# Kernel optimization log

Measured on AMD Instinct MI355X. Metric: run time of the kernel, lower is better.

The kernel has to match this reference:

```python
import jax, jax.numpy as jnp
import numpy as np

B, D, H = 4096, 64, 1024  # batch, state dim, hidden width


def setup_inputs() -> dict:
    key = jax.random.key(0)
    ks = jax.random.split(key, 4)
    def w(k, shape, fan_in):
        return (jax.random.normal(k, shape, jnp.float32) / np.float32(np.sqrt(fan_in)))
    return {
        "x": jax.random.normal(ks[0], (B, 1 + D), jnp.float32),
        "W1": w(ks[1], (D, H), D),
        "b1": jnp.zeros((H,), jnp.float32),
        "W2": w(ks[2], (H, H), H),
        "b2": jnp.zeros((H,), jnp.float32),
        "W3": w(ks[3], (H, D), H),
        "b3": jnp.zeros((D,), jnp.float32),
    }


def _mlp(z, W1, b1, W2, b2, W3, b3):
    # tanh MLP vector field: d -> h -> h -> d
    h = jnp.tanh(z @ W1 + b1)
    h = jnp.tanh(h @ W2 + b2)
    return h @ W3 + b3


def reference(x, W1, b1, W2, b2, W3, b3):
    x_in = x[:, 1:]                        # [B, D] state (col 0 is logp channel)
    f = lambda z: _mlp(z, W1, b1, W2, b2, W3, b3)
    x_out = f(x_in)                        # [B, D]

    # Exact Jacobian trace: same math as the torch per-dim autograd.grad loop,
    # expressed as D forward-mode JVPs vmapped over the identity basis.
    eye = jnp.eye(x_in.shape[1], dtype=x.dtype)

    def diag_entry(e):                     # e: [D] basis vector
        _, t = jax.jvp(f, (x_in,), (jnp.broadcast_to(e, x_in.shape),))
        return t @ e                       # [B] = J[:, i, i]

    trJ = jnp.sum(jax.vmap(diag_entry)(eye), axis=0)  # [B]

    out = jnp.concatenate([-trJ[:, None], x_out], axis=1)  # [B, 1+D]
    return out + 0.0 * x  # faithful to `+ 0 * x` in the original
```

## Files before the change

### kernel.cpp

```cpp
#include <hip/hip_runtime.h>
#include <cmath>

typedef unsigned short u16;
typedef __attribute__((ext_vector_type(8))) short s8v;
typedef __attribute__((ext_vector_type(4))) float f4v;
typedef __attribute__((ext_vector_type(16))) float f16v;

__device__ __forceinline__ u16 f2bf(float f) {
    union { float f; unsigned u; } v; v.f = f;
    unsigned r = v.u + 0x7FFFu + ((v.u >> 16) & 1u);
    return (u16)(r >> 16);
}
__device__ __forceinline__ float tanh_fast(float x) {
    float e = __builtin_amdgcn_exp2f(x * 2.88539008177792681f);
    return 1.f - 2.f * __builtin_amdgcn_rcpf(1.f + e);
}
__device__ __forceinline__ int wslot(int row, int c) {
    return ((((c >> 2) << 6) | ((c & 3) << 4) | (row & 15)) ^ c);
}
__device__ __forceinline__ size_t fragoff(int n, int k) {
    return (((size_t)(n >> 5) * 64 + (k >> 4)) * 64 + (n & 31) + (((k >> 3) & 1) << 5)) * 8 + (k & 7);
}

__launch_bounds__(256)
__global__ void cnf_prep(const float* __restrict__ x, const float* __restrict__ W1,
                         const float* __restrict__ W2, const float* __restrict__ W3,
                         u16* __restrict__ W2Tf, u16* __restrict__ VTf,
                         u16* __restrict__ xb, u16* __restrict__ W1T,
                         u16* __restrict__ W3Tf, float* __restrict__ trJ)
{
    __shared__ float w2s[32][33];
    __shared__ float w1s[32][68];
    const int a = blockIdx.x * 32;
    const int b = blockIdx.y * 32;
    const int t = threadIdx.x;

    #pragma unroll
    for (int it = 0; it < 4; ++it) {
        int idx = t + it * 256;
        w2s[idx >> 5][idx & 31] = W2[(a + (idx >> 5)) * 1024 + b + (idx & 31)];
    }
    #pragma unroll
    for (int it = 0; it < 8; ++it) {
        int idx = t + it * 256;
        w1s[idx & 31][idx >> 5] = W1[(idx >> 5) * 1024 + a + (idx & 31)];
    }
    __syncthreads();

    #pragma unroll
    for (int it = 0; it < 4; ++it) {
        int idx = t + it * 256;
        int rr = idx >> 5, cc = idx & 31;
        W2Tf[fragoff(b + rr, a + cc)] = f2bf(w2s[cc][rr]);
    }
    #pragma unroll
    for (int it = 0; it < 4; ++it) {
        int idx = t + it * 256;
        int qq = idx >> 5, pp = idx & 31;
        const float* w3row = W3 + (b + qq) * 64;
        float u = 0.f;
        #pragma unroll
        for (int i4 = 0; i4 < 16; ++i4) {
            f4v wv  = *(const f4v*)&w1s[pp][i4 * 4];
            f4v w3v = *(const f4v*)&w3row[i4 * 4];
            u += wv[0]*w3v[0] + wv[1]*w3v[1] + wv[2]*w3v[2] + wv[3]*w3v[3];
        }
        VTf[fragoff(b + qq, a + pp)] = f2bf(w2s[pp][qq] * u);
    }
    {
        int bid = blockIdx.y * 32 + blockIdx.x;
        int e = bid * 256 + t;
        xb[e] = f2bf(x[(e >> 6) * 65 + 1 + (e & 63)]);
    }
    if (blockIdx.y == 0) {
        int pp = t >> 3, i0 = (t & 7) * 8;
        s8v v;
        #pragma unroll
        for (int j = 0; j < 8; ++j) v[j] = (short)f2bf(w1s[pp][i0 + j]);
        *(s8v*)&W1T[(a + pp) * 64 + i0] = v;
        if (t < 128) trJ[blockIdx.x * 128 + t] = 0.f;
    }
    if (blockIdx.y == 1) {
        int idx = blockIdx.x * 256 + t;
        int n = idx & 63, k0 = (idx >> 6) * 8;
        s8v v;
        #pragma unroll
        for (int j = 0; j < 8; ++j) v[j] = (short)f2bf(W3[(k0 + j) * 64 + n]);
        *(s8v*)&W3Tf[fragoff(n, k0)] = v;
    }
}

__launch_bounds__(256)
__global__ void cnf_gemm1(const u16* __restrict__ xb, const u16* __restrict__ W1T,
                          const float* __restrict__ b1,
                          u16* __restrict__ h1, u16* __restrict__ g1)
{
    __shared__ __align__(16) u16 lds[12 * 1024];
    const int t = threadIdx.x;
    const int wave = t >> 6, lane = t & 63;
    const int wm = wave >> 1, wn = wave & 1;
    const int g = lane >> 4, lr = lane & 15;
    const int arow0 = blockIdx.x * 128, bcol0 = blockIdx.y * 64;

    #pragma unroll
    for (int i = 0; i < 4; ++i) {
        int ch = t + i * 256, row = ch >> 3, c = ch & 7;
        *(s8v*)&lds[(row >> 4) * 1024 + wslot(row, c) * 8] =
            *(const s8v*)&xb[(arow0 + row) * 64 + c * 8];
    }
    #pragma unroll
    for (int i = 0; i < 2; ++i) {
        int ch = t + i * 256, row = ch >> 3, c = ch & 7;
        *(s8v*)&lds[(8 + (row >> 4)) * 1024 + wslot(row, c) * 8] =
            *(const s8v*)&W1T[(bcol0 + row) * 64 + c * 8];
    }
    __syncthreads();

    f4v acc[4][2];
    #pragma unroll
    for (int mi = 0; mi < 4; ++mi)
        #pragma unroll
        for (int ni = 0; ni < 2; ++ni) acc[mi][ni] = f4v{0.f,0.f,0.f,0.f};

    #pragma unroll
    for (int ks = 0; ks < 2; ++ks) {
        const int lo = (ks * 64 + (lane ^ ((ks * 4 + g) & 7))) * 8;
        s8v af[4], bf[2];
        #pragma unroll
        for (int mi = 0; mi < 4; ++mi) af[mi] = *(const s8v*)&lds[(wm * 4 + mi) * 1024 + lo];
        #pragma unroll
        for (int ni = 0; ni < 2; ++ni) bf[ni] = *(const s8v*)&lds[(8 + wn * 2 + ni) * 1024 + lo];
        #pragma unroll
        for (int mi = 0; mi < 4; ++mi)
            #pragma unroll
            for (int ni = 0; ni < 2; ++ni)
                acc[mi][ni] = __builtin_amdgcn_mfma_f32_16x16x32_bf16(af[mi], bf[ni], acc[mi][ni], 0, 0, 0);
    }

    #pragma unroll
    for (int mi = 0; mi < 4; ++mi) {
        const int rowb = arow0 + wm * 64 + mi * 16 + g * 4;
        #pragma unroll
        for (int ni = 0; ni < 2; ++ni) {
            const int col = bcol0 + wn * 32 + ni * 16 + lr;
            const float bv = b1[col];
            #pragma unroll
            for (int r = 0; r < 4; ++r) {
                float h = tanh_fast(acc[mi][ni][r] + bv);
                h1[(rowb + r) * 1024 + col] = f2bf(h);
                g1[(rowb + r) * 1024 + col] = f2bf(1.f - h * h);
            }
        }
    }
}

#define LOADA(d0, d1, d2, d3, ko)                                              \
    do { d0 = *(const s8v*)(h1p0 + (ko)); d1 = *(const s8v*)(h1p1 + (ko));     \
         d2 = *(const s8v*)(g1p0 + (ko)); d3 = *(const s8v*)(g1p1 + (ko)); } while (0)

#define LOADB(B, kkg)                                                          \
    do { _Pragma("unroll")                                                     \
         for (int _ks = 0; _ks < 2; ++_ks)                                     \
         _Pragma("unroll")                                                     \
         for (int _ni = 0; _ni < 2; ++_ni) {                                   \
             size_t _o = (((size_t)(ntb + wn * 2 + _ni) * 64 + (kkg)*2 + _ks) * 64 + lane) * 8; \
             B[_ks*4 + _ni*2 + 0] = *(const s8v*)&W2Tf[_o];                    \
             B[_ks*4 + _ni*2 + 1] = *(const s8v*)&VTf[_o];                     \
         } } while (0)

#define WRITEA(s0, s1, s2, s3, bb)                                             \
    do { u16* _wb = &lds[bb][0];                                               \
         *(s8v*)&_wb[sdst0] = s0; *(s8v*)&_wb[sdst1] = s1;                     \
         *(s8v*)&_wb[4096 + sdst0] = s2; *(s8v*)&_wb[4096 + sdst1] = s3; } while (0)

#define MIDBODY(kt, Aw0, Aw1, Aw2, Aw3, Al0, Al1, Al2, Al3, Bc, Bn)            \
    {                                                                          \
        if ((kt) < 30) { const int _ko = ((kt) + 2) * 32;                      \
                         LOADA(Al0, Al1, Al2, Al3, _ko); }                     \
        if ((kt) < 31) { WRITEA(Aw0, Aw1, Aw2, Aw3, ((kt) + 1) & 1);           \
                         LOADB(Bn, (kt) + 1); }                                \
        const u16* buf = &lds[(kt) & 1][0];                                    \
        _Pragma("unroll")                                                      \
        for (int ks = 0; ks < 2; ++ks) {                                       \
            const int lp = (lane ^ ((lane >> 5) << 2) ^ (ks << 1)) * 8;        \
            s8v af1[2], af2[2];                                                \
            _Pragma("unroll")                                                  \
            for (int mi = 0; mi < 2; ++mi) {                                   \
                int R = (wm * 2 + mi) * 2 + ks;                                \
                af1[mi] = *(const s8v*)&buf[R * 512 + lp];                     \
                af2[mi] = *(const s8v*)&buf[4096 + R * 512 + lp];              \
            }                                                                  \
            _Pragma("unroll")                                                  \
            for (int mi = 0; mi < 2; ++mi)                                     \
                _Pragma("unroll")                                              \
                for (int ni = 0; ni < 2; ++ni) {                               \
                    acc1[mi][ni] = __builtin_amdgcn_mfma_f32_32x32x16_bf16(af1[mi], Bc[ks*4+ni*2+0], acc1[mi][ni], 0, 0, 0); \
                    acc2[mi][ni] = __builtin_amdgcn_mfma_f32_32x32x16_bf16(af2[mi], Bc[ks*4+ni*2+1], acc2[mi][ni], 0, 0, 0); \
                }                                                              \
        }                                                                      \
        __syncthreads();                                                       \
    }

__launch_bounds__(256, 1)
__global__ void cnf_mid(const u16* __restrict__ h1, const u16* __restrict__ g1,
                        const u16* __restrict__ W2Tf, const u16* __restrict__ VTf,
                        const float* __restrict__ b2,
                        u16* __restrict__ h2f, float* __restrict__ trJ)
{
    __shared__ __align__(16) u16 lds[2][8192];

    const int t = threadIdx.x;
    const int wave = t >> 6, lane = t & 63;
    const int wm = wave >> 1, wn = wave & 1;
    const int arow0 = blockIdx.x * 128;
    const int ntb = blockIdx.y * 4;

    const int row0 = t >> 2,        c0 = t & 3;
    const int row1 = (t + 256) >> 2, c1 = t & 3;
    int R0 = (row0 >> 5) * 2 + (c0 >> 1), L0 = (row0 & 31) + ((c0 & 1) << 5);
    int R1 = (row1 >> 5) * 2 + (c1 >> 1), L1 = (row1 & 31) + ((c1 & 1) << 5);
    const int sdst0 = (R0 * 64 + (L0 ^ ((L0 >> 5) << 2) ^ ((R0 & 1) << 1))) * 8;
    const int sdst1 = (R1 * 64 + (L1 ^ ((L1 >> 5) << 2) ^ ((R1 & 1) << 1))) * 8;
    const u16* h1p0 = h1 + (size_t)(arow0 + row0) * 1024 + c0 * 8;
    const u16* h1p1 = h1 + (size_t)(arow0 + row1) * 1024 + c1 * 8;
    const u16* g1p0 = g1 + (size_t)(arow0 + row0) * 1024 + c0 * 8;
    const u16* g1p1 = g1 + (size_t)(arow0 + row1) * 1024 + c1 * 8;

    f16v acc1[2][2], acc2[2][2];
    #pragma unroll
    for (int mi = 0; mi < 2; ++mi)
        #pragma unroll
        for (int ni = 0; ni < 2; ++ni) {
            #pragma unroll
            for (int r = 0; r < 16; ++r) { acc1[mi][ni][r] = 0.f; acc2[mi][ni][r] = 0.f; }
        }

    s8v aA0, aA1, aA2, aA3, aB0, aB1, aB2, aB3;
    s8v bA[8], bB[8];

    LOADA(aA0, aA1, aA2, aA3, 0);
    WRITEA(aA0, aA1, aA2, aA3, 0);
    LOADA(aB0, aB1, aB2, aB3, 32);
    LOADB(bA, 0);
    __syncthreads();

    for (int kt2 = 0; kt2 < 16; ++kt2) {
        const int kt = kt2 * 2;
        MIDBODY(kt,     aB0, aB1, aB2, aB3, aA0, aA1, aA2, aA3, bA, bB);
        MIDBODY(kt + 1, aA0, aA1, aA2, aA3, aB0, aB1, aB2, aB3, bB, bA);
    }

    const int l31 = lane & 31, lh = lane >> 5;
    #pragma unroll
    for (int mi = 0; mi < 2; ++mi) {
        const int rt = (arow0 >> 5) + wm * 2 + mi;
        float tr[16];
        #pragma unroll
        for (int r = 0; r < 16; ++r) tr[r] = 0.f;
        #pragma unroll
        for (int ni = 0; ni < 2; ++ni) {
            const int q0 = (ntb + wn * 2 + ni) * 32;
            const float bv = b2[q0 + l31];
            const size_t hb = (((size_t)rt * 64 + ((q0 + l31) >> 4)) * 64
                               + (((l31 >> 3) & 1) << 5)) * 8 + (l31 & 7) + lh * 32;
            #pragma unroll
            for (int r = 0; r < 16; ++r) {
                float hh = tanh_fast(acc1[mi][ni][r] + bv);
                float gg = 1.f - hh * hh;
                h2f[hb + ((r & 3) + ((r >> 2) << 3)) * 8] = f2bf(hh);
                tr[r] += acc2[mi][ni][r] * gg;
            }
        }
        #pragma unroll
        for (int off = 1; off < 32; off <<= 1)
            #pragma unroll
            for (int r = 0; r < 16; ++r) tr[r] += __shfl_xor(tr[r], off);
        if (l31 == 0) {
            const int rowb = arow0 + wm * 64 + mi * 32 + lh * 4;
            #pragma unroll
            for (int r = 0; r < 16; ++r)
                atomicAdd(&trJ[rowb + (r & 3) + ((r >> 2) << 3)], tr[r]);
        }
    }
}

__launch_bounds__(256)
__global__ void cnf_out(const u16* __restrict__ h2f, const u16* __restrict__ W3Tf,
                        const float* __restrict__ b3, const float* __restrict__ trJ,
                        float* __restrict__ out)
{
    __shared__ float red[4][32][64];
    const int t = threadIdx.x;
    const int wave = t >> 6, lane = t & 63;
    const int rt = blockIdx.x;

    f16v acc[2];
    #pragma unroll
    for (int ni = 0; ni < 2; ++ni)
        #pragma unroll
        for (int r = 0; r < 16; ++r) acc[ni][r] = 0.f;

    #pragma unroll
    for (int kki = 0; kki < 16; ++kki) {
        const int kk = wave * 16 + kki;
        s8v af = *(const s8v*)&h2f[(((size_t)rt * 64 + kk) * 64 + lane) * 8];
        #pragma unroll
        for (int ni = 0; ni < 2; ++ni) {
            s8v bf = *(const s8v*)&W3Tf[(((size_t)ni * 64 + kk) * 64 + lane) * 8];
            acc[ni] = __builtin_amdgcn_mfma_f32_32x32x16_bf16(af, bf, acc[ni], 0, 0, 0);
        }
    }
    const int l31 = lane & 31, lh = lane >> 5;
    #pragma unroll
    for (int ni = 0; ni < 2; ++ni)
        #pragma unroll
        for (int r = 0; r < 16; ++r)
            red[wave][(r & 3) + ((r >> 2) << 3) + lh * 4][ni * 32 + l31] = acc[ni][r];
    __syncthreads();

    #pragma unroll
    for (int i = 0; i < 8; ++i) {
        int o = t * 8 + i;
        int row = o >> 6, col = o & 63;
        float s = red[0][row][col] + red[1][row][col] + red[2][row][col] + red[3][row][col] + b3[col];
        out[(size_t)(rt * 32 + row) * 65 + 1 + col] = s;
    }
    if (t < 32) out[(size_t)(rt * 32 + t) * 65] = -trJ[rt * 32 + t];
}

extern "C" void kernel_launch(void* const* d_in, const int* in_sizes, int n_in,
                              void* d_out, int out_size, void* d_ws, size_t ws_size,
                              hipStream_t stream) {
    const float* x  = (const float*)d_in[0];
    const float* W1 = (const float*)d_in[1];
    const float* b1 = (const float*)d_in[2];
    const float* W2 = (const float*)d_in[3];
    const float* b2 = (const float*)d_in[4];
    const float* W3 = (const float*)d_in[5];
    const float* b3 = (const float*)d_in[6];
    float* out = (float*)d_out;

    char* ws = (char*)d_ws;
    u16*   h1b = (u16*)(ws);
    u16*   g1b = (u16*)(ws + (size_t)( 8u << 20));
    u16*   h2f = (u16*)(ws + (size_t)(16u << 20));
    u16*   W2T = (u16*)(ws + (size_t)(24u << 20));
    u16*   VTb = (u16*)(ws + (size_t)(26u << 20));
    float* trJ = (float*)(ws + (size_t)(28u << 20));
    u16*   xbb = (u16*)(ws + (size_t)(28u << 20) + 65536);
    u16*   W1T = (u16*)(ws + (size_t)(28u << 20) + 65536 + 524288);
    u16*   W3T = (u16*)(ws + (size_t)(28u << 20) + 65536 + 524288 + 131072);

    cnf_prep <<<dim3(32, 32), 256, 0, stream>>>(x, W1, W2, W3, W2T, VTb, xbb, W1T, W3T, trJ);
    cnf_gemm1<<<dim3(32, 16), 256, 0, stream>>>(xbb, W1T, b1, h1b, g1b);
    cnf_mid  <<<dim3(32, 8),  256, 0, stream>>>(h1b, g1b, W2T, VTb, b2, h2f, trJ);
    cnf_out  <<<128,          256, 0, stream>>>(h2f, W3T, b3, trJ, out);
}
```

Measured before the change: 61.29 us.

## Store h1/g1 in MFMA fragment layout and drop LDS staging in mid GEMM

gemm1 now stages its tanh outputs in swizzled LDS and writes h1/g1 to global memory in pre-tiled MFMA fragment order with 16-byte vector stores, replacing scalar row-major stores. cnf_mid then loads A and B fragments straight from global memory each k-step, with no LDS double buffering and no barriers. The aim is to cut LDS traffic and sync overhead in the main GEMM and to make the gemm1 stores coalesced. The cost is that mid no longer prefetches explicitly, so it depends on cache hits and compiler scheduling (unroll 4) to hide global load latency.

```diff
diff --git a/kernel.cpp b/kernel.cpp
--- a/kernel.cpp
+++ b/kernel.cpp
@@ -93,9 +93,11 @@
 __launch_bounds__(256)
 __global__ void cnf_gemm1(const u16* __restrict__ xb, const u16* __restrict__ W1T,
                           const float* __restrict__ b1,
-                          u16* __restrict__ h1, u16* __restrict__ g1)
+                          u16* __restrict__ h1f, u16* __restrict__ g1f)
 {
     __shared__ __align__(16) u16 lds[12 * 1024];
+    __shared__ __align__(16) u16 hls[128 * 64];
+    __shared__ __align__(16) u16 gls[128 * 64];
     const int t = threadIdx.x;
     const int wave = t >> 6, lane = t & 63;
     const int wm = wave >> 1, wn = wave & 1;
@@ -139,115 +141,94 @@
 
     #pragma unroll
     for (int mi = 0; mi < 4; ++mi) {
-        const int rowb = arow0 + wm * 64 + mi * 16 + g * 4;
+        const int rowl = wm * 64 + mi * 16 + g * 4;
         #pragma unroll
         for (int ni = 0; ni < 2; ++ni) {
-            const int col = bcol0 + wn * 32 + ni * 16 + lr;
-            const float bv = b1[col];
+            const int coll = wn * 32 + ni * 16 + lr;
+            const float bv = b1[bcol0 + coll];
+            const int cc = coll >> 3, jj = coll & 7;
             #pragma unroll
             for (int r = 0; r < 4; ++r) {
+                const int row = rowl + r;
                 float h = tanh_fast(acc[mi][ni][r] + bv);
-                h1[(rowb + r) * 1024 + col] = f2bf(h);
-                g1[(rowb + r) * 1024 + col] = f2bf(1.f - h * h);
+                int idx = row * 64 + ((cc ^ (row & 7)) << 3) + jj;
+                hls[idx] = f2bf(h);
+                gls[idx] = f2bf(1.f - h * h);
             }
         }
     }
-}
-
-#define LOADA(d0, d1, d2, d3, ko)                                              \
-    do { d0 = *(const s8v*)(h1p0 + (ko)); d1 = *(const s8v*)(h1p1 + (ko));     \
-         d2 = *(const s8v*)(g1p0 + (ko)); d3 = *(const s8v*)(g1p1 + (ko)); } while (0)
-
-#define LOADB(B, kkg)                                                          \
-    do { _Pragma("unroll")                                                     \
-         for (int _ks = 0; _ks < 2; ++_ks)                                     \
-         _Pragma("unroll")                                                     \
-         for (int _ni = 0; _ni < 2; ++_ni) {                                   \
-             size_t _o = (((size_t)(ntb + wn * 2 + _ni) * 64 + (kkg)*2 + _ks) * 64 + lane) * 8; \
-             B[_ks*4 + _ni*2 + 0] = *(const s8v*)&W2Tf[_o];                    \
-             B[_ks*4 + _ni*2 + 1] = *(const s8v*)&VTf[_o];                     \
-         } } while (0)
-
-#define WRITEA(s0, s1, s2, s3, bb)                                             \
-    do { u16* _wb = &lds[bb][0];                                               \
-         *(s8v*)&_wb[sdst0] = s0; *(s8v*)&_wb[sdst1] = s1;                     \
-         *(s8v*)&_wb[4096 + sdst0] = s2; *(s8v*)&_wb[4096 + sdst1] = s3; } while (0)
-
-#define MIDBODY(kt, Aw0, Aw1, Aw2, Aw3, Al0, Al1, Al2, Al3, Bc, Bn)            \
-    {                                                                          \
-        if ((kt) < 30) { const int _ko = ((kt) + 2) * 32;                      \
-                         LOADA(Al0, Al1, Al2, Al3, _ko); }                     \
-        if ((kt) < 31) { WRITEA(Aw0, Aw1, Aw2, Aw3, ((kt) + 1) & 1);           \
-                         LOADB(Bn, (kt) + 1); }                                \
-        const u16* buf = &lds[(kt) & 1][0];                                    \
-        _Pragma("unroll")                                                      \
-        for (int ks = 0; ks < 2; ++ks) {                                       \
-            const int lp = (lane ^ ((lane >> 5) << 2) ^ (ks << 1)) * 8;        \
-            s8v af1[2], af2[2];                                                \
-            _Pragma("unroll")                                                  \
-            for (int mi = 0; mi < 2; ++mi) {                                   \
-                int R = (wm * 2 + mi) * 2 + ks;                                \
-                af1[mi] = *(const s8v*)&buf[R * 512 + lp];                     \
-                af2[mi] = *(const s8v*)&buf[4096 + R * 512 + lp];              \
-            }                                                                  \
-            _Pragma("unroll")                                                  \
-            for (int mi = 0; mi < 2; ++mi)                                     \
-                _Pragma("unroll")                                              \
-                for (int ni = 0; ni < 2; ++ni) {                               \
-                    acc1[mi][ni] = __builtin_amdgcn_mfma_f32_32x32x16_bf16(af1[mi], Bc[ks*4+ni*2+0], acc1[mi][ni], 0, 0, 0); \
-                    acc2[mi][ni] = __builtin_amdgcn_mfma_f32_32x32x16_bf16(af2[mi], Bc[ks*4+ni*2+1], acc2[mi][ni], 0, 0, 0); \
-                }                                                              \
-        }                                                                      \
-        __syncthreads();                                                       \
-    }
+    __syncthreads();
+
+    const int rt0 = arow0 >> 5, kk0 = bcol0 >> 4;
+    #pragma unroll
+    for (int i = 0; i < 4; ++i) {
+        const int tile = (i * 256 + t) >> 6;
+        const int ln = t & 63;
+        const int rt = tile >> 2, kk = tile & 3;
+        const int row = rt * 32 + (ln & 31);
+        const int kb = kk * 16 + (ln >> 5) * 8;
+        const int src = row * 64 + (((kb >> 3) ^ (row & 7)) << 3);
+        const size_t dst = ((size_t)(rt0 + rt) * 64 + (kk0 + kk)) * 512 + ln * 8;
+        *(s8v*)&h1f[dst] = *(const s8v*)&hls[src];
+        *(s8v*)&g1f[dst] = *(const s8v*)&gls[src];
+    }
+}
 
 __launch_bounds__(256, 1)
-__global__ void cnf_mid(const u16* __restrict__ h1, const u16* __restrict__ g1,
+__global__ void cnf_mid(const u16* __restrict__ h1f, const u16* __restrict__ g1f,
                         const u16* __restrict__ W2Tf, const u16* __restrict__ VTf,
                         const float* __restrict__ b2,
                         u16* __restrict__ h2f, float* __restrict__ trJ)
 {
-    __shared__ __align__(16) u16 lds[2][8192];
-
     const int t = threadIdx.x;
     const int wave = t >> 6, lane = t & 63;
     const int wm = wave >> 1, wn = wave & 1;
     const int arow0 = blockIdx.x * 128;
     const int ntb = blockIdx.y * 4;
-
-    const int row0 = t >> 2,        c0 = t & 3;
-    const int row1 = (t + 256) >> 2, c1 = t & 3;
-    int R0 = (row0 >> 5) * 2 + (c0 >> 1), L0 = (row0 & 31) + ((c0 & 1) << 5);
-    int R1 = (row1 >> 5) * 2 + (c1 >> 1), L1 = (row1 & 31) + ((c1 & 1) << 5);
-    const int sdst0 = (R0 * 64 + (L0 ^ ((L0 >> 5) << 2) ^ ((R0 & 1) << 1))) * 8;
-    const int sdst1 = (R1 * 64 + (L1 ^ ((L1 >> 5) << 2) ^ ((R1 & 1) << 1))) * 8;
-    const u16* h1p0 = h1 + (size_t)(arow0 + row0) * 1024 + c0 * 8;
-    const u16* h1p1 = h1 + (size_t)(arow0 + row1) * 1024 + c1 * 8;
-    const u16* g1p0 = g1 + (size_t)(arow0 + row0) * 1024 + c0 * 8;
-    const u16* g1p1 = g1 + (size_t)(arow0 + row1) * 1024 + c1 * 8;
+    const int rt0 = (arow0 >> 5) + wm * 2;
+    const int nt0 = ntb + wn * 2;
+
+    const u16* pa1[2], *pa2[2], *pb1[2], *pb2[2];
+    #pragma unroll
+    for (int mi = 0; mi < 2; ++mi) {
+        pa1[mi] = h1f + (size_t)(rt0 + mi) * 64 * 512 + lane * 8;
+        pa2[mi] = g1f + (size_t)(rt0 + mi) * 64 * 512 + lane * 8;
+    }
+    #pragma unroll
+    for (int ni = 0; ni < 2; ++ni) {
+        pb1[ni] = W2Tf + (size_t)(nt0 + ni) * 64 * 512 + lane * 8;
+        pb2[ni] = VTf  + (size_t)(nt0 + ni) * 64 * 512 + lane * 8;
+    }
 
     f16v acc1[2][2], acc2[2][2];
     #pragma unroll
     for (int mi = 0; mi < 2; ++mi)
         #pragma unroll
+        for (int ni = 0; ni < 2; ++ni)
+            #pragma unroll
+            for (int r = 0; r < 16; ++r) { acc1[mi][ni][r] = 0.f; acc2[mi][ni][r] = 0.f; }
+
+    #pragma unroll 4
+    for (int kk = 0; kk < 64; ++kk) {
+        const size_t o = (size_t)kk * 512;
+        s8v a1[2], a2[2], b1f[2], b2f[2];
+        #pragma unroll
+        for (int mi = 0; mi < 2; ++mi) {
+            a1[mi] = *(const s8v*)(pa1[mi] + o);
+            a2[mi] = *(const s8v*)(pa2[mi] + o);
+        }
+        #pragma unroll
         for (int ni = 0; ni < 2; ++ni) {
-            #pragma unroll
-            for (int r = 0; r < 16; ++r) { acc1[mi][ni][r] = 0.f; acc2[mi][ni][r] = 0.f; }
-        }
-
-    s8v aA0, aA1, aA2, aA3, aB0, aB1, aB2, aB3;
-    s8v bA[8], bB[8];
-
-    LOADA(aA0, aA1, aA2, aA3, 0);
-    WRITEA(aA0, aA1, aA2, aA3, 0);
-    LOADA(aB0, aB1, aB2, aB3, 32);
-    LOADB(bA, 0);
-    __syncthreads();
-
-    for (int kt2 = 0; kt2 < 16; ++kt2) {
-        const int kt = kt2 * 2;
-        MIDBODY(kt,     aB0, aB1, aB2, aB3, aA0, aA1, aA2, aA3, bA, bB);
-        MIDBODY(kt + 1, aA0, aA1, aA2, aA3, aB0, aB1, aB2, aB3, bB, bA);
+            b1f[ni] = *(const s8v*)(pb1[ni] + o);
+            b2f[ni] = *(const s8v*)(pb2[ni] + o);
+        }
+        #pragma unroll
+        for (int mi = 0; mi < 2; ++mi)
+            #pragma unroll
+            for (int ni = 0; ni < 2; ++ni) {
+                acc1[mi][ni] = __builtin_amdgcn_mfma_f32_32x32x16_bf16(a1[mi], b1f[ni], acc1[mi][ni], 0, 0, 0);
+                acc2[mi][ni] = __builtin_amdgcn_mfma_f32_32x32x16_bf16(a2[mi], b2f[ni], acc2[mi][ni], 0, 0, 0);
+            }
     }
 
     const int l31 = lane & 31, lh = lane >> 5;
@@ -341,8 +322,8 @@
     float* out = (float*)d_out;
 
     char* ws = (char*)d_ws;
-    u16*   h1b = (u16*)(ws);
-    u16*   g1b = (u16*)(ws + (size_t)( 8u << 20));
+    u16*   h1f = (u16*)(ws);
+    u16*   g1f = (u16*)(ws + (size_t)( 8u << 20));
     u16*   h2f = (u16*)(ws + (size_t)(16u << 20));
     u16*   W2T = (u16*)(ws + (size_t)(24u << 20));
     u16*   VTb = (u16*)(ws + (size_t)(26u << 20));
@@ -352,7 +333,7 @@
     u16*   W3T = (u16*)(ws + (size_t)(28u << 20) + 65536 + 524288 + 131072);
 
     cnf_prep <<<dim3(32, 32), 256, 0, stream>>>(x, W1, W2, W3, W2T, VTb, xbb, W1T, W3T, trJ);
-    cnf_gemm1<<<dim3(32, 16), 256, 0, stream>>>(xbb, W1T, b1, h1b, g1b);
-    cnf_mid  <<<dim3(32, 8),  256, 0, stream>>>(h1b, g1b, W2T, VTb, b2, h2f, trJ);
+    cnf_gemm1<<<dim3(32, 16), 256, 0, stream>>>(xbb, W1T, b1, h1f, g1f);
+    cnf_mid  <<<dim3(32, 8),  256, 0, stream>>>(h1f, g1f, W2T, VTb, b2, h2f, trJ);
     cnf_out  <<<128,          256, 0, stream>>>(h2f, W3T, b3, trJ, out);
 }
```

Measured after the change: 65.47 us. +6.8%, slower.

## Split mid GEMM across 8 waves, stage gemm1 epilogue in LDS, fix prep layout

Applied to the files above, without the earlier changes.

The mid kernel moves from 4 waves of 256 threads, each owning a 2x2 tile of 32x32 MFMA blocks, to 8 waves of 512 threads, each owning a 1x2 tile. This halves accumulator registers per wave and allows two blocks per CU (launch bounds 512,2), trading fewer registers per wave for more latency hiding. gemm1 now writes h1/g1 into swizzled LDS first and then stores 16-byte vectors, replacing scattered 2-byte global stores. The prep kernel's W1 shared tile is transposed to a padded [64][33] layout to cut bank conflicts, at the cost of replacing vector LDS reads with scalar ones.

```diff
diff --git a/kernel.cpp b/kernel.cpp
--- a/kernel.cpp
+++ b/kernel.cpp
@@ -30,7 +30,7 @@
                          u16* __restrict__ W3Tf, float* __restrict__ trJ)
 {
     __shared__ float w2s[32][33];
-    __shared__ float w1s[32][68];
+    __shared__ float w1s[64][33];
     const int a = blockIdx.x * 32;
     const int b = blockIdx.y * 32;
     const int t = threadIdx.x;
@@ -43,7 +43,7 @@
     #pragma unroll
     for (int it = 0; it < 8; ++it) {
         int idx = t + it * 256;
-        w1s[idx & 31][idx >> 5] = W1[(idx >> 5) * 1024 + a + (idx & 31)];
+        w1s[idx >> 5][idx & 31] = W1[(idx >> 5) * 1024 + a + (idx & 31)];
     }
     __syncthreads();
 
@@ -61,9 +61,9 @@
         float u = 0.f;
         #pragma unroll
         for (int i4 = 0; i4 < 16; ++i4) {
-            f4v wv  = *(const f4v*)&w1s[pp][i4 * 4];
             f4v w3v = *(const f4v*)&w3row[i4 * 4];
-            u += wv[0]*w3v[0] + wv[1]*w3v[1] + wv[2]*w3v[2] + wv[3]*w3v[3];
+            u += w3v[0] * w1s[i4 * 4 + 0][pp] + w3v[1] * w1s[i4 * 4 + 1][pp]
+               + w3v[2] * w1s[i4 * 4 + 2][pp] + w3v[3] * w1s[i4 * 4 + 3][pp];
         }
         VTf[fragoff(b + qq, a + pp)] = f2bf(w2s[pp][qq] * u);
     }
@@ -76,7 +76,7 @@
         int pp = t >> 3, i0 = (t & 7) * 8;
         s8v v;
         #pragma unroll
-        for (int j = 0; j < 8; ++j) v[j] = (short)f2bf(w1s[pp][i0 + j]);
+        for (int j = 0; j < 8; ++j) v[j] = (short)f2bf(w1s[i0 + j][pp]);
         *(s8v*)&W1T[(a + pp) * 64 + i0] = v;
         if (t < 128) trJ[blockIdx.x * 128 + t] = 0.f;
     }
@@ -96,6 +96,8 @@
                           u16* __restrict__ h1, u16* __restrict__ g1)
 {
     __shared__ __align__(16) u16 lds[12 * 1024];
+    __shared__ __align__(16) u16 hls[128 * 64];
+    __shared__ __align__(16) u16 gls[128 * 64];
     const int t = threadIdx.x;
     const int wave = t >> 6, lane = t & 63;
     const int wm = wave >> 1, wn = wave & 1;
@@ -139,69 +141,73 @@
 
     #pragma unroll
     for (int mi = 0; mi < 4; ++mi) {
-        const int rowb = arow0 + wm * 64 + mi * 16 + g * 4;
+        const int rowl = wm * 64 + mi * 16 + g * 4;
         #pragma unroll
         for (int ni = 0; ni < 2; ++ni) {
-            const int col = bcol0 + wn * 32 + ni * 16 + lr;
-            const float bv = b1[col];
+            const int coll = wn * 32 + ni * 16 + lr;
+            const float bv = b1[bcol0 + coll];
+            const int cc = coll >> 3, jj = coll & 7;
             #pragma unroll
             for (int r = 0; r < 4; ++r) {
+                const int row = rowl + r;
                 float h = tanh_fast(acc[mi][ni][r] + bv);
-                h1[(rowb + r) * 1024 + col] = f2bf(h);
-                g1[(rowb + r) * 1024 + col] = f2bf(1.f - h * h);
+                int idx = row * 64 + ((cc ^ (row & 7)) << 3) + jj;
+                hls[idx] = f2bf(h);
+                gls[idx] = f2bf(1.f - h * h);
             }
         }
     }
-}
-
-#define LOADA(d0, d1, d2, d3, ko)                                              \
-    do { d0 = *(const s8v*)(h1p0 + (ko)); d1 = *(const s8v*)(h1p1 + (ko));     \
-         d2 = *(const s8v*)(g1p0 + (ko)); d3 = *(const s8v*)(g1p1 + (ko)); } while (0)
+    __syncthreads();
+
+    #pragma unroll
+    for (int i = 0; i < 4; ++i) {
+        int id = i * 256 + t;
+        int row = id >> 3, ch = id & 7;
+        int src = row * 64 + ((ch ^ (row & 7)) << 3);
+        size_t dst = (size_t)(arow0 + row) * 1024 + bcol0 + ch * 8;
+        *(s8v*)&h1[dst] = *(const s8v*)&hls[src];
+        *(s8v*)&g1[dst] = *(const s8v*)&gls[src];
+    }
+}
+
+#define LOADA(dh, dg, ko) \
+    do { dh = *(const s8v*)(h1p + (ko)); dg = *(const s8v*)(g1p + (ko)); } while (0)
 
 #define LOADB(B, kkg)                                                          \
     do { _Pragma("unroll")                                                     \
          for (int _ks = 0; _ks < 2; ++_ks)                                     \
          _Pragma("unroll")                                                     \
          for (int _ni = 0; _ni < 2; ++_ni) {                                   \
-             size_t _o = (((size_t)(ntb + wn * 2 + _ni) * 64 + (kkg)*2 + _ks) * 64 + lane) * 8; \
+             size_t _o = (((size_t)(nt0 + _ni) * 64 + (kkg) * 2 + _ks) * 64 + lane) * 8; \
              B[_ks*4 + _ni*2 + 0] = *(const s8v*)&W2Tf[_o];                    \
              B[_ks*4 + _ni*2 + 1] = *(const s8v*)&VTf[_o];                     \
          } } while (0)
 
-#define WRITEA(s0, s1, s2, s3, bb)                                             \
+#define WRITEA(sh, sg, bb)                                                     \
     do { u16* _wb = &lds[bb][0];                                               \
-         *(s8v*)&_wb[sdst0] = s0; *(s8v*)&_wb[sdst1] = s1;                     \
-         *(s8v*)&_wb[4096 + sdst0] = s2; *(s8v*)&_wb[4096 + sdst1] = s3; } while (0)
-
-#define MIDBODY(kt, Aw0, Aw1, Aw2, Aw3, Al0, Al1, Al2, Al3, Bc, Bn)            \
+         *(s8v*)&_wb[sdst] = sh; *(s8v*)&_wb[4096 + sdst] = sg; } while (0)
+
+#define MIDBODY(kt, AwH, AwG, AlH, AlG, Bc, Bn)                                \
     {                                                                          \
-        if ((kt) < 30) { const int _ko = ((kt) + 2) * 32;                      \
-                         LOADA(Al0, Al1, Al2, Al3, _ko); }                     \
-        if ((kt) < 31) { WRITEA(Aw0, Aw1, Aw2, Aw3, ((kt) + 1) & 1);           \
-                         LOADB(Bn, (kt) + 1); }                                \
+        if ((kt) < 30) { const int _ko = ((kt) + 2) * 32; LOADA(AlH, AlG, _ko); } \
+        if ((kt) < 31) { WRITEA(AwH, AwG, ((kt) + 1) & 1); LOADB(Bn, (kt) + 1); } \
         const u16* buf = &lds[(kt) & 1][0];                                    \
         _Pragma("unroll")                                                      \
         for (int ks = 0; ks < 2; ++ks) {                                       \
             const int lp = (lane ^ ((lane >> 5) << 2) ^ (ks << 1)) * 8;        \
-            s8v af1[2], af2[2];                                                \
+            const int R = wrt * 2 + ks;                                        \
+            s8v a1 = *(const s8v*)&buf[R * 512 + lp];                          \
+            s8v a2 = *(const s8v*)&buf[4096 + R * 512 + lp];                   \
             _Pragma("unroll")                                                  \
-            for (int mi = 0; mi < 2; ++mi) {                                   \
-                int R = (wm * 2 + mi) * 2 + ks;                                \
-                af1[mi] = *(const s8v*)&buf[R * 512 + lp];                     \
-                af2[mi] = *(const s8v*)&buf[4096 + R * 512 + lp];              \
+            for (int ni = 0; ni < 2; ++ni) {                                   \
+                acc1[ni] = __builtin_amdgcn_mfma_f32_32x32x16_bf16(a1, Bc[ks*4+ni*2+0], acc1[ni], 0, 0, 0); \
+                acc2[ni] = __builtin_amdgcn_mfma_f32_32x32x16_bf16(a2, Bc[ks*4+ni*2+1], acc2[ni], 0, 0, 0); \
             }                                                                  \
-            _Pragma("unroll")                                                  \
-            for (int mi = 0; mi < 2; ++mi)                                     \
-                _Pragma("unroll")                                              \
-                for (int ni = 0; ni < 2; ++ni) {                               \
-                    acc1[mi][ni] = __builtin_amdgcn_mfma_f32_32x32x16_bf16(af1[mi], Bc[ks*4+ni*2+0], acc1[mi][ni], 0, 0, 0); \
-                    acc2[mi][ni] = __builtin_amdgcn_mfma_f32_32x32x16_bf16(af2[mi], Bc[ks*4+ni*2+1], acc2[mi][ni], 0, 0, 0); \
-                }                                                              \
         }                                                                      \
         __syncthreads();                                                       \
     }
 
-__launch_bounds__(256, 1)
+__launch_bounds__(512, 2)
 __global__ void cnf_mid(const u16* __restrict__ h1, const u16* __restrict__ g1,
                         const u16* __restrict__ W2Tf, const u16* __restrict__ VTf,
                         const float* __restrict__ b2,
@@ -211,76 +217,68 @@
 
     const int t = threadIdx.x;
     const int wave = t >> 6, lane = t & 63;
-    const int wm = wave >> 1, wn = wave & 1;
+    const int wrt = wave & 3;
+    const int wn  = wave >> 2;
     const int arow0 = blockIdx.x * 128;
     const int ntb = blockIdx.y * 4;
-
-    const int row0 = t >> 2,        c0 = t & 3;
-    const int row1 = (t + 256) >> 2, c1 = t & 3;
-    int R0 = (row0 >> 5) * 2 + (c0 >> 1), L0 = (row0 & 31) + ((c0 & 1) << 5);
-    int R1 = (row1 >> 5) * 2 + (c1 >> 1), L1 = (row1 & 31) + ((c1 & 1) << 5);
-    const int sdst0 = (R0 * 64 + (L0 ^ ((L0 >> 5) << 2) ^ ((R0 & 1) << 1))) * 8;
-    const int sdst1 = (R1 * 64 + (L1 ^ ((L1 >> 5) << 2) ^ ((R1 & 1) << 1))) * 8;
-    const u16* h1p0 = h1 + (size_t)(arow0 + row0) * 1024 + c0 * 8;
-    const u16* h1p1 = h1 + (size_t)(arow0 + row1) * 1024 + c1 * 8;
-    const u16* g1p0 = g1 + (size_t)(arow0 + row0) * 1024 + c0 * 8;
-    const u16* g1p1 = g1 + (size_t)(arow0 + row1) * 1024 + c1 * 8;
-
-    f16v acc1[2][2], acc2[2][2];
-    #pragma unroll
-    for (int mi = 0; mi < 2; ++mi)
-        #pragma unroll
-        for (int ni = 0; ni < 2; ++ni) {
-            #pragma unroll
-            for (int r = 0; r < 16; ++r) { acc1[mi][ni][r] = 0.f; acc2[mi][ni][r] = 0.f; }
-        }
-
-    s8v aA0, aA1, aA2, aA3, aB0, aB1, aB2, aB3;
+    const int nt0 = ntb + wn * 2;
+
+    const int row = t >> 2, c = t & 3;
+    const int R0 = (row >> 5) * 2 + (c >> 1);
+    const int L0 = (row & 31) + ((c & 1) << 5);
+    const int sdst = (R0 * 64 + (L0 ^ ((L0 >> 5) << 2) ^ ((R0 & 1) << 1))) * 8;
+    const u16* h1p = h1 + (size_t)(arow0 + row) * 1024 + c * 8;
+    const u16* g1p = g1 + (size_t)(arow0 + row) * 1024 + c * 8;
+
+    f16v acc1[2], acc2[2];
+    #pragma unroll
+    for (int ni = 0; ni < 2; ++ni)
+        #pragma unroll
+        for (int r = 0; r < 16; ++r) { acc1[ni][r] = 0.f; acc2[ni][r] = 0.f; }
+
+    s8v ahA, agA, ahB, agB;
     s8v bA[8], bB[8];
 
-    LOADA(aA0, aA1, aA2, aA3, 0);
-    WRITEA(aA0, aA1, aA2, aA3, 0);
-    LOADA(aB0, aB1, aB2, aB3, 32);
+    LOADA(ahA, agA, 0);
+    WRITEA(ahA, agA, 0);
+    LOADA(ahB, agB, 32);
     LOADB(bA, 0);
     __syncthreads();
 
     for (int kt2 = 0; kt2 < 16; ++kt2) {
         const int kt = kt2 * 2;
-        MIDBODY(kt,     aB0, aB1, aB2, aB3, aA0, aA1, aA2, aA3, bA, bB);
-        MIDBODY(kt + 1, aA0, aA1, aA2, aA3, aB0, aB1, aB2, aB3, bB, bA);
+        MIDBODY(kt,     ahB, agB, ahA, agA, bA, bB);
+        MIDBODY(kt + 1, ahA, agA, ahB, agB, bB, bA);
     }
 
     const int l31 = lane & 31, lh = lane >> 5;
-    #pragma unroll
-    for (int mi = 0; mi < 2; ++mi) {
-        const int rt = (arow0 >> 5) + wm * 2 + mi;
-        float tr[16];
-        #pragma unroll
-        for (int r = 0; r < 16; ++r) tr[r] = 0.f;
-        #pragma unroll
-        for (int ni = 0; ni < 2; ++ni) {
-            const int q0 = (ntb + wn * 2 + ni) * 32;
-            const float bv = b2[q0 + l31];
-            const size_t hb = (((size_t)rt * 64 + ((q0 + l31) >> 4)) * 64
-                               + (((l31 >> 3) & 1) << 5)) * 8 + (l31 & 7) + lh * 32;
-            #pragma unroll
-            for (int r = 0; r < 16; ++r) {
-                float hh = tanh_fast(acc1[mi][ni][r] + bv);
-                float gg = 1.f - hh * hh;
-                h2f[hb + ((r & 3) + ((r >> 2) << 3)) * 8] = f2bf(hh);
-                tr[r] += acc2[mi][ni][r] * gg;
-            }
+    const int rt = (arow0 >> 5) + wrt;
+    float tr[16];
+    #pragma unroll
+    for (int r = 0; r < 16; ++r) tr[r] = 0.f;
+    #pragma unroll
+    for (int ni = 0; ni < 2; ++ni) {
+        const int q0 = (nt0 + ni) * 32;
+        const float bv = b2[q0 + l31];
+        const size_t hb = (((size_t)rt * 64 + ((q0 + l31) >> 4)) * 64
+                           + (((l31 >> 3) & 1) << 5)) * 8 + (l31 & 7) + lh * 32;
+        #pragma unroll
+        for (int r = 0; r < 16; ++r) {
+            float hh = tanh_fast(acc1[ni][r] + bv);
+            float gg = 1.f - hh * hh;
+            h2f[hb + ((r & 3) + ((r >> 2) << 3)) * 8] = f2bf(hh);
+            tr[r] += acc2[ni][r] * gg;
         }
-        #pragma unroll
-        for (int off = 1; off < 32; off <<= 1)
-            #pragma unroll
-            for (int r = 0; r < 16; ++r) tr[r] += __shfl_xor(tr[r], off);
-        if (l31 == 0) {
-            const int rowb = arow0 + wm * 64 + mi * 32 + lh * 4;
-            #pragma unroll
-            for (int r = 0; r < 16; ++r)
-                atomicAdd(&trJ[rowb + (r & 3) + ((r >> 2) << 3)], tr[r]);
-        }
+    }
+    #pragma unroll
+    for (int off = 1; off < 32; off <<= 1)
+        #pragma unroll
+        for (int r = 0; r < 16; ++r) tr[r] += __shfl_xor(tr[r], off);
+    if (l31 == 0) {
+        const int rowb = arow0 + wrt * 32 + lh * 4;
+        #pragma unroll
+        for (int r = 0; r < 16; ++r)
+            atomicAdd(&trJ[rowb + (r & 3) + ((r >> 2) << 3)], tr[r]);
     }
 }
 
@@ -353,6 +351,6 @@
 
     cnf_prep <<<dim3(32, 32), 256, 0, stream>>>(x, W1, W2, W3, W2T, VTb, xbb, W1T, W3T, trJ);
     cnf_gemm1<<<dim3(32, 16), 256, 0, stream>>>(xbb, W1T, b1, h1b, g1b);
-    cnf_mid  <<<dim3(32, 8),  256, 0, stream>>>(h1b, g1b, W2T, VTb, b2, h2f, trJ);
+    cnf_mid  <<<dim3(32, 8),  512, 0, stream>>>(h1b, g1b, W2T, VTb, b2, h2f, trJ);
     cnf_out  <<<128,          256, 0, stream>>>(h2f, W3T, b3, trJ, out);
 }
```

Result: no change. 61.54 us (+0.4%).
